# Optimization experiments

Hardware: AMD Instinct MI355X
Metric: run time of the kernel (lower is better)

## Reference

```python
import jax, jax.numpy as jnp
import numpy as np

N_NODES = 100000
N_EDGES = 1600000
N_FEAT = 128
N_CLASSES = 10
N_GRAPHS = 256


def setup_inputs() -> dict:
    key = jax.random.key(0)
    ks = jax.random.split(key, 16)
    x = jax.random.normal(ks[0], (N_NODES, N_FEAT), dtype=jnp.float32)
    edge_index = jax.random.randint(ks[1], (2, N_EDGES), 0, N_NODES, dtype=jnp.int64)
    batch = jnp.sort(jax.random.randint(ks[2], (N_NODES,), 0, N_GRAPHS, dtype=jnp.int64))
    s = 0.1
    # GAT1: in=128 -> heads=8, out_per_head=8, concat -> 64
    W1 = jax.random.normal(ks[3], (N_FEAT, 64), dtype=jnp.float32) * s
    a_src1 = jax.random.normal(ks[4], (8, 8), dtype=jnp.float32) * s
    a_dst1 = jax.random.normal(ks[5], (8, 8), dtype=jnp.float32) * s
    b1 = jnp.zeros((64,), jnp.float32)
    # GAT2: in=64 -> heads=1, out=128
    W2 = jax.random.normal(ks[6], (64, 128), dtype=jnp.float32) * s
    a_src2 = jax.random.normal(ks[7], (1, 128), dtype=jnp.float32) * s
    a_dst2 = jax.random.normal(ks[8], (1, 128), dtype=jnp.float32) * s
    b2 = jnp.zeros((128,), jnp.float32)
    fc_w = jax.random.normal(ks[9], (128, N_CLASSES), dtype=jnp.float32) * s
    fc_b = jnp.zeros((N_CLASSES,), jnp.float32)
    return {"x": x, "edge_index": edge_index, "batch": batch,
            "W1": W1, "a_src1": a_src1, "a_dst1": a_dst1, "b1": b1,
            "W2": W2, "a_src2": a_src2, "a_dst2": a_dst2, "b2": b2,
            "fc_w": fc_w, "fc_b": fc_b}


def _segment_softmax(e, seg, n):
    # e: [E, H]; softmax over edges sharing the same destination node
    m = jax.ops.segment_max(e, seg, num_segments=n)
    m = jnp.where(jnp.isfinite(m), m, jnp.zeros_like(m))  # guard isolated nodes
    ex = jnp.exp(e - m[seg])
    s = jax.ops.segment_sum(ex, seg, num_segments=n)
    return ex / (s[seg] + jnp.asarray(1e-16, e.dtype))


def _gat_conv(x, src, dst, W, a_src, a_dst, bias):
    # PyG GATConv (eval mode, self-loops already appended to src/dst)
    H, C = a_src.shape
    n = x.shape[0]
    h = (x @ W).reshape(n, H, C)                      # [N,H,C]
    al_s = jnp.einsum('nhc,hc->nh', h, a_src)          # [N,H]
    al_d = jnp.einsum('nhc,hc->nh', h, a_dst)
    e = jax.nn.leaky_relu(al_s[src] + al_d[dst], 0.2)  # [E,H]
    alpha = _segment_softmax(e, dst, n)                # [E,H]
    out = jax.ops.segment_sum(h[src] * alpha[..., None], dst, num_segments=n)  # [N,H,C]
    return out.reshape(n, H * C) + bias                # concat=True (H=1 layer2 is identity reshape)


def reference(x, edge_index, batch, W1, a_src1, a_dst1, b1, W2, a_src2, a_dst2, b2, fc_w, fc_b):
    n = x.shape[0]
    loop = jnp.arange(n, dtype=edge_index.dtype)
    src = jnp.concatenate([edge_index[0], loop])       # add self-loops (PyG default)
    dst = jnp.concatenate([edge_index[1], loop])
    x1 = jax.nn.relu(_gat_conv(x, src, dst, W1, a_src1, a_dst1, b1))
    # dropout p=0.6 is identity in eval mode
    x2 = _gat_conv(x1, src, dst, W2, a_src2, a_dst2, b2)
    cnt = jax.ops.segment_sum(jnp.ones((n,), x2.dtype), batch, num_segments=N_GRAPHS)
    pooled = jax.ops.segment_sum(x2, batch, num_segments=N_GRAPHS) / jnp.maximum(cnt, 1.0)[:, None]
    logits = pooled @ fc_w + fc_b
    return jax.nn.log_softmax(logits, axis=1)
```

## Files before the change

kernel.cpp:

```cpp
#include <hip/hip_runtime.h>
#include <math.h>

typedef unsigned int uint;
typedef unsigned short ushort;
typedef unsigned char uchar;
typedef __attribute__((ext_vector_type(2))) float v2f;
typedef __attribute__((ext_vector_type(4))) _Float16 h4v;
typedef __attribute__((ext_vector_type(8))) _Float16 h8v;

#define S1 4.0f
#define S2 16.0f

template <bool HI>
__device__ inline v2f fp8x2f(uint u) {
    return __builtin_amdgcn_cvt_pk_f32_fp8((int)u, HI);
}

__global__ __launch_bounds__(256) void k_g1h(const float* __restrict__ x,
                                             const float* __restrict__ W1,
                                             const float* __restrict__ as1,
                                             const float* __restrict__ ad1,
                                             uchar* __restrict__ rec1,
                                             const int* __restrict__ dst,
                                             int* __restrict__ counts,
                                             int N, int E, int CH, int NB, int GB) {
    __shared__ float sB[128 * 64];
    __shared__ float sA[64 * 68];
    const int t = threadIdx.x;
    if (blockIdx.x >= GB) {
        int b = blockIdx.x - GB;
        int* hist = (int*)sB;
        for (int k = t; k < NB; k += 256) hist[k] = 0;
        __syncthreads();
        int e0 = b * CH;
        int e1 = e0 + CH; if (e1 > E) e1 = E;
        for (int e = e0 + t; e < e1; e += 256)
            atomicAdd(&hist[dst[e] >> 7], 1);
        __syncthreads();
        for (int k = t; k < NB; k += 256) counts[(size_t)b * NB + k] = hist[k];
        return;
    }
    const int n0 = blockIdx.x * 64;
    {
        const float4* w4 = (const float4*)W1;
        float4* s4 = (float4*)sB;
#pragma unroll
        for (int i = 0; i < 8; ++i) s4[t + i * 256] = w4[t + i * 256];
    }
    const int r0 = (t >> 3) * 2;
    const int c0 = (t & 7) * 8;
    float acc0[8] = {0, 0, 0, 0, 0, 0, 0, 0};
    float acc1[8] = {0, 0, 0, 0, 0, 0, 0, 0};
    for (int kb = 0; kb < 2; ++kb) {
        __syncthreads();
#pragma unroll
        for (int i = 0; i < 4; ++i) {
            int idx = t + i * 256;
            int r = idx >> 4, kc = idx & 15;
            int n = n0 + r;
            float4 v = make_float4(0.f, 0.f, 0.f, 0.f);
            if (n < N) v = ((const float4*)x)[(size_t)n * 32 + kb * 16 + kc];
            *(float4*)&sA[r * 68 + kc * 4] = v;
        }
        __syncthreads();
        const float* bptr = &sB[kb * 64 * 64];
#pragma unroll 8
        for (int kk = 0; kk < 64; ++kk) {
            float a0 = sA[r0 * 68 + kk];
            float a1 = sA[(r0 + 1) * 68 + kk];
            const float* bp = &bptr[kk * 64 + c0];
            float4 b0 = *(const float4*)bp;
            float4 b1v = *(const float4*)(bp + 4);
            acc0[0] += a0 * b0.x; acc0[1] += a0 * b0.y; acc0[2] += a0 * b0.z; acc0[3] += a0 * b0.w;
            acc0[4] += a0 * b1v.x; acc0[5] += a0 * b1v.y; acc0[6] += a0 * b1v.z; acc0[7] += a0 * b1v.w;
            acc1[0] += a1 * b0.x; acc1[1] += a1 * b0.y; acc1[2] += a1 * b0.z; acc1[3] += a1 * b0.w;
            acc1[4] += a1 * b1v.x; acc1[5] += a1 * b1v.y; acc1[6] += a1 * b1v.z; acc1[7] += a1 * b1v.w;
        }
    }
    float ps0 = 0.f, pd0 = 0.f, ps1 = 0.f, pd1 = 0.f;
#pragma unroll
    for (int i = 0; i < 8; ++i) {
        float ws = as1[c0 + i], wd = ad1[c0 + i];
        ps0 += acc0[i] * ws; pd0 += acc0[i] * wd;
        ps1 += acc1[i] * ws; pd1 += acc1[i] * wd;
    }
    int n = n0 + r0;
    int head = t & 7;
    if (n < N) {
        int q0 = 0, q1 = 0;
        q0 = __builtin_amdgcn_cvt_pk_fp8_f32(acc0[0] * S1, acc0[1] * S1, q0, false);
        q0 = __builtin_amdgcn_cvt_pk_fp8_f32(acc0[2] * S1, acc0[3] * S1, q0, true);
        q1 = __builtin_amdgcn_cvt_pk_fp8_f32(acc0[4] * S1, acc0[5] * S1, q1, false);
        q1 = __builtin_amdgcn_cvt_pk_fp8_f32(acc0[6] * S1, acc0[7] * S1, q1, true);
        uint2 p; p.x = (uint)q0; p.y = (uint)q1;
        uchar* rp = rec1 + (size_t)n * 128;
        *(uint2*)(rp + c0) = p;
        *(float*)(rp + 64 + head * 4) = ps0;
        *(float*)(rp + 96 + head * 4) = pd0;
    }
    if (n + 1 < N) {
        int q0 = 0, q1 = 0;
        q0 = __builtin_amdgcn_cvt_pk_fp8_f32(acc1[0] * S1, acc1[1] * S1, q0, false);
        q0 = __builtin_amdgcn_cvt_pk_fp8_f32(acc1[2] * S1, acc1[3] * S1, q0, true);
        q1 = __builtin_amdgcn_cvt_pk_fp8_f32(acc1[4] * S1, acc1[5] * S1, q1, false);
        q1 = __builtin_amdgcn_cvt_pk_fp8_f32(acc1[6] * S1, acc1[7] * S1, q1, true);
        uint2 p; p.x = (uint)q0; p.y = (uint)q1;
        uchar* rp = rec1 + (size_t)(n + 1) * 128;
        *(uint2*)(rp + c0) = p;
        *(float*)(rp + 64 + head * 4) = ps1;
        *(float*)(rp + 96 + head * 4) = pd1;
    }
}

__global__ __launch_bounds__(256) void k_gemm2(const _Float16* __restrict__ x1pre,
                                               const float* __restrict__ W2,
                                               const float* __restrict__ b1,
                                               const float* __restrict__ as2,
                                               const float* __restrict__ ad2,
                                               uchar* __restrict__ h2f8,
                                               float* __restrict__ al2s,
                                               float* __restrict__ al2d, int N) {
    __shared__ float sB[64 * 128];
    __shared__ float sA[64 * 68];
    const int t = threadIdx.x;
    const int n0 = blockIdx.x * 64;
    {
        const float4* w4 = (const float4*)W2;
        float4* s4 = (float4*)sB;
#pragma unroll
        for (int i = 0; i < 8; ++i) s4[t + i * 256] = w4[t + i * 256];
    }
#pragma unroll
    for (int i = 0; i < 4; ++i) {
        int idx = t + i * 256;
        int r = idx >> 4, kc = idx & 15;
        int n = n0 + r;
        float4 v = make_float4(0.f, 0.f, 0.f, 0.f);
        if (n < N) {
            h4v hv = *(const h4v*)(x1pre + (size_t)n * 64 + kc * 4);
            float4 bb = ((const float4*)b1)[kc];
            v.x = fmaxf((float)hv[0] + bb.x, 0.f);
            v.y = fmaxf((float)hv[1] + bb.y, 0.f);
            v.z = fmaxf((float)hv[2] + bb.z, 0.f);
            v.w = fmaxf((float)hv[3] + bb.w, 0.f);
        }
        *(float4*)&sA[r * 68 + kc * 4] = v;
    }
    __syncthreads();
    const int r0 = (t >> 3) * 2;
    const int cb = (t & 7) * 4;
    float acc0[16], acc1[16];
#pragma unroll
    for (int i = 0; i < 16; ++i) { acc0[i] = 0.f; acc1[i] = 0.f; }
#pragma unroll 4
    for (int k = 0; k < 64; ++k) {
        float a0 = sA[r0 * 68 + k];
        float a1 = sA[(r0 + 1) * 68 + k];
#pragma unroll
        for (int j = 0; j < 4; ++j) {
            float4 b = *(const float4*)&sB[k * 128 + cb + 32 * j];
            acc0[j * 4 + 0] += a0 * b.x; acc0[j * 4 + 1] += a0 * b.y;
            acc0[j * 4 + 2] += a0 * b.z; acc0[j * 4 + 3] += a0 * b.w;
            acc1[j * 4 + 0] += a1 * b.x; acc1[j * 4 + 1] += a1 * b.y;
            acc1[j * 4 + 2] += a1 * b.z; acc1[j * 4 + 3] += a1 * b.w;
        }
    }
    float ps0 = 0.f, pd0 = 0.f, ps1 = 0.f, pd1 = 0.f;
#pragma unroll
    for (int j = 0; j < 4; ++j)
#pragma unroll
        for (int i = 0; i < 4; ++i) {
            int cc = cb + 32 * j + i;
            float ws = as2[cc], wd = ad2[cc];
            ps0 += acc0[j * 4 + i] * ws; pd0 += acc0[j * 4 + i] * wd;
            ps1 += acc1[j * 4 + i] * ws; pd1 += acc1[j * 4 + i] * wd;
        }
#pragma unroll
    for (int off = 1; off < 8; off <<= 1) {
        ps0 += __shfl_xor(ps0, off); pd0 += __shfl_xor(pd0, off);
        ps1 += __shfl_xor(ps1, off); pd1 += __shfl_xor(pd1, off);
    }
    int n = n0 + r0;
    if (n < N) {
#pragma unroll
        for (int j = 0; j < 4; ++j) {
            int q = 0;
            q = __builtin_amdgcn_cvt_pk_fp8_f32(acc0[j * 4 + 0] * S2, acc0[j * 4 + 1] * S2, q, false);
            q = __builtin_amdgcn_cvt_pk_fp8_f32(acc0[j * 4 + 2] * S2, acc0[j * 4 + 3] * S2, q, true);
            *(uint*)&h2f8[(size_t)n * 128 + cb + 32 * j] = (uint)q;
        }
        if ((t & 7) == 0) { al2s[n] = ps0; al2d[n] = pd0; }
    }
    if (n + 1 < N) {
#pragma unroll
        for (int j = 0; j < 4; ++j) {
            int q = 0;
            q = __builtin_amdgcn_cvt_pk_fp8_f32(acc1[j * 4 + 0] * S2, acc1[j * 4 + 1] * S2, q, false);
            q = __builtin_amdgcn_cvt_pk_fp8_f32(acc1[j * 4 + 2] * S2, acc1[j * 4 + 3] * S2, q, true);
            *(uint*)&h2f8[(size_t)(n + 1) * 128 + cb + 32 * j] = (uint)q;
        }
        if ((t & 7) == 0) { al2s[n + 1] = ps1; al2d[n + 1] = pd1; }
    }
}


__global__ __launch_bounds__(256) void k_bscan(int* __restrict__ counts,
                                               int* __restrict__ btot,
                                               int C, int NB) {
    __shared__ int sh[256];
    int t = threadIdx.x, k = blockIdx.x;
    int v[4];
#pragma unroll
    for (int i = 0; i < 4; ++i) {
        int b = t * 4 + i;
        v[i] = (b < C) ? counts[(size_t)b * NB + k] : 0;
    }
    int s = v[0] + v[1] + v[2] + v[3];
    sh[t] = s;
    __syncthreads();
    int accv = s;
    for (int off = 1; off < 256; off <<= 1) {
        int u = (t >= off) ? sh[t - off] : 0;
        __syncthreads();
        accv += u;
        sh[t] = accv;
        __syncthreads();
    }
    int excl = accv - s;
#pragma unroll
    for (int i = 0; i < 4; ++i) {
        int b = t * 4 + i;
        if (b < C) counts[(size_t)b * NB + k] = excl;
        excl += v[i];
    }
    if (t == 255) btot[k] = accv;
}

__global__ __launch_bounds__(256) void k_bucket(const int* __restrict__ src,
                                                const int* __restrict__ dst,
                                                const int* __restrict__ counts,
                                                const int* __restrict__ btot,
                                                int* __restrict__ bbase,
                                                int* __restrict__ ebuf,
                                                int E, int CH, int NB) {
    __shared__ int pos[784];
    __shared__ int sh[256];
    __shared__ int bb[784];
    int t = threadIdx.x, b = blockIdx.x;
    int v[4];
#pragma unroll
    for (int i = 0; i < 4; ++i) {
        int k = t * 4 + i;
        v[i] = (k < NB) ? btot[k] : 0;
    }
    int s = v[0] + v[1] + v[2] + v[3];
    sh[t] = s;
    __syncthreads();
    int accv = s;
    for (int off = 1; off < 256; off <<= 1) {
        int u = (t >= off) ? sh[t - off] : 0;
        __syncthreads();
        accv += u;
        sh[t] = accv;
        __syncthreads();
    }
    int excl = accv - s;
#pragma unroll
    for (int i = 0; i < 4; ++i) {
        int k = t * 4 + i;
        if (k < NB) bb[k] = excl;
        excl += v[i];
    }
    __syncthreads();
    for (int k = t; k < NB; k += 256)
        pos[k] = bb[k] + counts[(size_t)b * NB + k];
    if (b == 0) {
        for (int k = t; k < NB; k += 256) bbase[k] = bb[k];
        if (t == 0) bbase[NB] = E;
    }
    __syncthreads();
    int e0 = b * CH;
    int e1 = e0 + CH; if (e1 > E) e1 = E;
    for (int e = e0 + t; e < e1; e += 256) {
        int d = dst[e], s2 = src[e];
        int p = atomicAdd(&pos[d >> 7], 1);
        ebuf[p] = (int)((uint)s2 | ((uint)(d & 127) << 25));
    }
}

__global__ __launch_bounds__(256) void k_csr(const int* __restrict__ bbase,
                                             const int* __restrict__ ebuf,
                                             int* __restrict__ row_ptr,
                                             int* __restrict__ col,
                                             int N, int E) {
    __shared__ int cnt[128];
    __shared__ int fill[128];
    __shared__ int rowb[128];
    __shared__ int sh[256];
    int t = threadIdx.x, k = blockIdx.x;
    int lo = bbase[k], hi = bbase[k + 1];
    int nlo = k << 7;
    int nn = N - nlo; if (nn > 128) nn = 128;
    if (t < 128) { cnt[t] = 0; fill[t] = 0; }
    __syncthreads();
    for (int i = lo + t; i < hi; i += 256)
        atomicAdd(&cnt[((uint)ebuf[i]) >> 25], 1);
    __syncthreads();
    int v = (t < nn) ? (cnt[t] + 1) : 0;
    sh[t] = v;
    __syncthreads();
    int accv = v;
    for (int off = 1; off < 256; off <<= 1) {
        int u = (t >= off) ? sh[t - off] : 0;
        __syncthreads();
        accv += u;
        sh[t] = accv;
        __syncthreads();
    }
    int fbase = lo + nlo;
    if (t < nn) {
        int rb = fbase + accv - v;
        rowb[t] = rb;
        row_ptr[nlo + t] = rb;
        col[rb + cnt[t]] = nlo + t;
    }
    if (k == 0 && t == 0) row_ptr[N] = E + N;
    __syncthreads();
    for (int i = lo + t; i < hi; i += 256) {
        uint e = (uint)ebuf[i];
        int j = (int)(e >> 25);
        int r = atomicAdd(&fill[j], 1);
        col[rowb[j] + r] = (int)(e & 0x1FFFFFFu);
    }
}

__global__ __launch_bounds__(256) void k_edge1(const uchar* __restrict__ rec1,
                                               const int* __restrict__ row_ptr,
                                               const int* __restrict__ col,
                                               _Float16* __restrict__ x1pre, int N) {
    int node = blockIdx.x * 4 + (threadIdx.x >> 6);
    if (node >= N) return;
    const int lane = threadIdx.x & 63;
    const int g = lane >> 4;
    const int k4 = lane & 15;
    const int hh = k4 >> 1;
    const uint co = (uint)(k4 * 4);
    const uint ao = 64u + (uint)(hh * 4);
    const float a_dh = *(const float*)(rec1 + (((size_t)node) << 7) + 96 + hh * 4);
    const int s0 = row_ptr[node], s1 = row_ptr[node + 1];
    float den_part = 0.f;
    v2f accL = {0.f, 0.f};
    v2f accH = {0.f, 0.f};
    for (int base = s0; base < s1; base += 64) {
        int cnt = s1 - base; if (cnt > 64) cnt = 64;
        int cntR = (cnt + 3) & ~3;
        int i = 0;
        for (; i + 16 <= cntR; i += 16) {
            int eA = base + i + g, eB = eA + 4, eC = eA + 8, eD = eA + 12;
            int xD = eD < s1 ? eD : s1 - 1;
            int cA = col[eA], cB = col[eB], cC = col[eC], cD = col[xD];
            const uchar* rA = rec1 + (((uint)cA) << 7);
            const uchar* rB = rec1 + (((uint)cB) << 7);
            const uchar* rC = rec1 + (((uint)cC) << 7);
            const uchar* rD = rec1 + (((uint)cD) << 7);
            uint hA = *(const uint*)(rA + co);
            uint hB = *(const uint*)(rB + co);
            uint hC = *(const uint*)(rC + co);
            uint hD = *(const uint*)(rD + co);
            float lA = *(const float*)(rA + ao) + a_dh;
            float lB = *(const float*)(rB + ao) + a_dh;
            float lC = *(const float*)(rC + ao) + a_dh;
            float lD = *(const float*)(rD + ao) + a_dh;
            lA = lA > 0.f ? lA : 0.2f * lA;
            lB = lB > 0.f ? lB : 0.2f * lB;
            lC = lC > 0.f ? lC : 0.2f * lC;
            lD = lD > 0.f ? lD : 0.2f * lD;
            float wA = __expf(lA);
            float wB = __expf(lB);
            float wC = __expf(lC);
            float wD = (eD < s1) ? __expf(lD) : 0.f;
            den_part += wA + wB + wC + wD;
            v2f wA2 = {wA, wA}, wB2 = {wB, wB}, wC2 = {wC, wC}, wD2 = {wD, wD};
            accL += wA2 * fp8x2f<false>(hA);
            accH += wA2 * fp8x2f<true>(hA);
            accL += wB2 * fp8x2f<false>(hB);
            accH += wB2 * fp8x2f<true>(hB);
            accL += wC2 * fp8x2f<false>(hC);
            accH += wC2 * fp8x2f<true>(hC);
            accL += wD2 * fp8x2f<false>(hD);
            accH += wD2 * fp8x2f<true>(hD);
        }
        int rem = cntR - i;
        if (rem & 8) {
            int eA = base + i + g, eB = eA + 4;
            int xB = eB < s1 ? eB : s1 - 1;
            int cA = col[eA], cB = col[xB];
            const uchar* rA = rec1 + (((uint)cA) << 7);
            const uchar* rB = rec1 + (((uint)cB) << 7);
            uint hA = *(const uint*)(rA + co);
            uint hB = *(const uint*)(rB + co);
            float lA = *(const float*)(rA + ao) + a_dh;
            float lB = *(const float*)(rB + ao) + a_dh;
            lA = lA > 0.f ? lA : 0.2f * lA;
            lB = lB > 0.f ? lB : 0.2f * lB;
            float wA = __expf(lA);
            float wB = (eB < s1) ? __expf(lB) : 0.f;
            den_part += wA + wB;
            v2f wA2 = {wA, wA}, wB2 = {wB, wB};
            accL += wA2 * fp8x2f<false>(hA);
            accH += wA2 * fp8x2f<true>(hA);
            accL += wB2 * fp8x2f<false>(hB);
            accH += wB2 * fp8x2f<true>(hB);
            i += 8;
        }
        if (rem & 4) {
            int eA = base + i + g;
            int xA = eA < s1 ? eA : s1 - 1;
            int cA = col[xA];
            const uchar* rA = rec1 + (((uint)cA) << 7);
            uint hA = *(const uint*)(rA + co);
            float lA = *(const float*)(rA + ao) + a_dh;
            lA = lA > 0.f ? lA : 0.2f * lA;
            float wA = (eA < s1) ? __expf(lA) : 0.f;
            den_part += wA;
            v2f wA2 = {wA, wA};
            accL += wA2 * fp8x2f<false>(hA);
            accH += wA2 * fp8x2f<true>(hA);
        }
    }
    float a0 = accL.x, a1 = accL.y, a2 = accH.x, a3 = accH.y;
    a0 += __shfl_xor(a0, 16); a0 += __shfl_xor(a0, 32);
    a1 += __shfl_xor(a1, 16); a1 += __shfl_xor(a1, 32);
    a2 += __shfl_xor(a2, 16); a2 += __shfl_xor(a2, 32);
    a3 += __shfl_xor(a3, 16); a3 += __shfl_xor(a3, 32);
    den_part += __shfl_xor(den_part, 16);
    den_part += __shfl_xor(den_part, 32);
    if (lane < 16) {
        float invd = 1.f / (den_part * S1);
        h4v o;
        o[0] = (_Float16)(a0 * invd);
        o[1] = (_Float16)(a1 * invd);
        o[2] = (_Float16)(a2 * invd);
        o[3] = (_Float16)(a3 * invd);
        *(h4v*)(x1pre + (size_t)node * 64 + co) = o;
    }
}

__global__ __launch_bounds__(256) void k_edge2(const uchar* __restrict__ h2f8,
                                               const float* __restrict__ al2s,
                                               const float* __restrict__ al2d,
                                               const int* __restrict__ row_ptr,
                                               const int* __restrict__ col,
                                               _Float16* __restrict__ x2, int N) {
    int node = blockIdx.x * 4 + (threadIdx.x >> 6);
    if (node >= N) return;
    const int lane = threadIdx.x & 63;
    const int g = lane >> 4;
    const int k8 = lane & 15;
    const uint co = (uint)(k8 * 8);
    const float a_d = al2d[node];
    const int s0 = row_ptr[node], s1 = row_ptr[node + 1];
    v2f acc0 = {0.f, 0.f}, acc1 = {0.f, 0.f}, acc2 = {0.f, 0.f}, acc3 = {0.f, 0.f};
    float den_part = 0.f;
    for (int base = s0; base < s1; base += 64) {
        int cnt = s1 - base; if (cnt > 64) cnt = 64;
        int cntR = (cnt + 3) & ~3;
        int i = 0;
        for (; i + 16 <= cntR; i += 16) {
            int eA = base + i + g, eB = eA + 4, eC = eA + 8, eD = eA + 12;
            int xD = eD < s1 ? eD : s1 - 1;
            int cA = col[eA], cB = col[eB], cC = col[eC], cD = col[xD];
            uint2 hA = *(const uint2*)(h2f8 + ((((uint)cA) << 7) | co));
            uint2 hB = *(const uint2*)(h2f8 + ((((uint)cB) << 7) | co));
            uint2 hC = *(const uint2*)(h2f8 + ((((uint)cC) << 7) | co));
            uint2 hD = *(const uint2*)(h2f8 + ((((uint)cD) << 7) | co));
            float lA = al2s[(uint)cA] + a_d;
            float lB = al2s[(uint)cB] + a_d;
            float lC = al2s[(uint)cC] + a_d;
            float lD = al2s[(uint)cD] + a_d;
            lA = lA > 0.f ? lA : 0.2f * lA;
            lB = lB > 0.f ? lB : 0.2f * lB;
            lC = lC > 0.f ? lC : 0.2f * lC;
            lD = lD > 0.f ? lD : 0.2f * lD;
            float wA = __expf(lA);
            float wB = __expf(lB);
            float wC = __expf(lC);
            float wD = (eD < s1) ? __expf(lD) : 0.f;
            den_part += wA + wB + wC + wD;
            v2f wA2 = {wA, wA}, wB2 = {wB, wB}, wC2 = {wC, wC}, wD2 = {wD, wD};
            acc0 += wA2 * fp8x2f<false>(hA.x);
            acc1 += wA2 * fp8x2f<true>(hA.x);
            acc2 += wA2 * fp8x2f<false>(hA.y);
            acc3 += wA2 * fp8x2f<true>(hA.y);
            acc0 += wB2 * fp8x2f<false>(hB.x);
            acc1 += wB2 * fp8x2f<true>(hB.x);
            acc2 += wB2 * fp8x2f<false>(hB.y);
            acc3 += wB2 * fp8x2f<true>(hB.y);
            acc0 += wC2 * fp8x2f<false>(hC.x);
            acc1 += wC2 * fp8x2f<true>(hC.x);
            acc2 += wC2 * fp8x2f<false>(hC.y);
            acc3 += wC2 * fp8x2f<true>(hC.y);
            acc0 += wD2 * fp8x2f<false>(hD.x);
            acc1 += wD2 * fp8x2f<true>(hD.x);
            acc2 += wD2 * fp8x2f<false>(hD.y);
            acc3 += wD2 * fp8x2f<true>(hD.y);
        }
        int rem = cntR - i;
        if (rem & 8) {
            int eA = base + i + g, eB = eA + 4;
            int xB = eB < s1 ? eB : s1 - 1;
            int cA = col[eA], cB = col[xB];
            uint2 hA = *(const uint2*)(h2f8 + ((((uint)cA) << 7) | co));
            uint2 hB = *(const uint2*)(h2f8 + ((((uint)cB) << 7) | co));
            float lA = al2s[(uint)cA] + a_d;
            float lB = al2s[(uint)cB] + a_d;
            lA = lA > 0.f ? lA : 0.2f * lA;
            lB = lB > 0.f ? lB : 0.2f * lB;
            float wA = __expf(lA);
            float wB = (eB < s1) ? __expf(lB) : 0.f;
            den_part += wA + wB;
            v2f wA2 = {wA, wA}, wB2 = {wB, wB};
            acc0 += wA2 * fp8x2f<false>(hA.x);
            acc1 += wA2 * fp8x2f<true>(hA.x);
            acc2 += wA2 * fp8x2f<false>(hA.y);
            acc3 += wA2 * fp8x2f<true>(hA.y);
            acc0 += wB2 * fp8x2f<false>(hB.x);
            acc1 += wB2 * fp8x2f<true>(hB.x);
            acc2 += wB2 * fp8x2f<false>(hB.y);
            acc3 += wB2 * fp8x2f<true>(hB.y);
            i += 8;
        }
        if (rem & 4) {
            int eA = base + i + g;
            int xA = eA < s1 ? eA : s1 - 1;
            int cA = col[xA];
            uint2 hA = *(const uint2*)(h2f8 + ((((uint)cA) << 7) | co));
            float lA = al2s[(uint)cA] + a_d;
            lA = lA > 0.f ? lA : 0.2f * lA;
            float wA = (eA < s1) ? __expf(lA) : 0.f;
            den_part += wA;
            v2f wA2 = {wA, wA};
            acc0 += wA2 * fp8x2f<false>(hA.x);
            acc1 += wA2 * fp8x2f<true>(hA.x);
            acc2 += wA2 * fp8x2f<false>(hA.y);
            acc3 += wA2 * fp8x2f<true>(hA.y);
        }
    }
    den_part += __shfl_xor(den_part, 16);
    den_part += __shfl_xor(den_part, 32);
    float r0 = acc0.x, r1 = acc0.y, r2 = acc1.x, r3 = acc1.y;
    float r4 = acc2.x, r5 = acc2.y, r6 = acc3.x, r7 = acc3.y;
    r0 += __shfl_xor(r0, 16); r0 += __shfl_xor(r0, 32);
    r1 += __shfl_xor(r1, 16); r1 += __shfl_xor(r1, 32);
    r2 += __shfl_xor(r2, 16); r2 += __shfl_xor(r2, 32);
    r3 += __shfl_xor(r3, 16); r3 += __shfl_xor(r3, 32);
    r4 += __shfl_xor(r4, 16); r4 += __shfl_xor(r4, 32);
    r5 += __shfl_xor(r5, 16); r5 += __shfl_xor(r5, 32);
    r6 += __shfl_xor(r6, 16); r6 += __shfl_xor(r6, 32);
    r7 += __shfl_xor(r7, 16); r7 += __shfl_xor(r7, 32);
    if (lane < 16) {
        float invd = 1.f / (den_part * S2);
        h8v o;
        o[0] = (_Float16)(r0 * invd);
        o[1] = (_Float16)(r1 * invd);
        o[2] = (_Float16)(r2 * invd);
        o[3] = (_Float16)(r3 * invd);
        o[4] = (_Float16)(r4 * invd);
        o[5] = (_Float16)(r5 * invd);
        o[6] = (_Float16)(r6 * invd);
        o[7] = (_Float16)(r7 * invd);
        *(h8v*)(x2 + (size_t)node * 128 + co) = o;
    }
}

__global__ __launch_bounds__(128) void k_poolfc(const _Float16* __restrict__ x2,
                                                const int* __restrict__ batch,
                                                const float* __restrict__ b2,
                                                const float* __restrict__ fcw,
                                                const float* __restrict__ fcb,
                                                float* __restrict__ out,
                                                int N, int G) {
    __shared__ float sp[128];
    const int g = blockIdx.x;
    const int t = threadIdx.x;
    int lo = 0, hi = N;
    while (lo < hi) { int m = (lo + hi) >> 1; if (batch[m] < g) lo = m + 1; else hi = m; }
    const int s = lo;
    hi = N;
    while (lo < hi) { int m = (lo + hi) >> 1; if (batch[m] < g + 1) lo = m + 1; else hi = m; }
    const int e = lo;
    float a0 = 0.f, a1 = 0.f, a2 = 0.f, a3 = 0.f;
    int n = s;
    for (; n + 4 <= e; n += 4) {
        a0 += (float)x2[(size_t)(n + 0) * 128 + t];
        a1 += (float)x2[(size_t)(n + 1) * 128 + t];
        a2 += (float)x2[(size_t)(n + 2) * 128 + t];
        a3 += (float)x2[(size_t)(n + 3) * 128 + t];
    }
    for (; n < e; ++n) a0 += (float)x2[(size_t)n * 128 + t];
    float inv = 1.f / fmaxf((float)(e - s), 1.f);
    sp[t] = (a0 + a1 + a2 + a3) * inv + b2[t];
    __syncthreads();
    if (t < 64) {
        int c = t;
        float2 p = ((const float2*)sp)[c];
        float l[10];
#pragma unroll
        for (int j = 0; j < 10; ++j)
            l[j] = p.x * fcw[(2 * c) * 10 + j] + p.y * fcw[(2 * c + 1) * 10 + j];
#pragma unroll
        for (int j = 0; j < 10; ++j)
            for (int off = 1; off < 64; off <<= 1) l[j] += __shfl_xor(l[j], off);
        if (c == 0) {
            float lj[10];
            float m = -1e30f;
#pragma unroll
            for (int j = 0; j < 10; ++j) {
                lj[j] = l[j] + fcb[j];
                m = fmaxf(m, lj[j]);
            }
            float sde = 0.f;
#pragma unroll
            for (int j = 0; j < 10; ++j) sde += expf(lj[j] - m);
            float ls = logf(sde);
#pragma unroll
            for (int j = 0; j < 10; ++j) out[(size_t)g * 10 + j] = lj[j] - m - ls;
        }
    }
}

extern "C" void kernel_launch(void* const* d_in, const int* in_sizes, int n_in,
                              void* d_out, int out_size, void* d_ws, size_t ws_size,
                              hipStream_t stream) {
    const float* x     = (const float*)d_in[0];
    const int*   ei    = (const int*)d_in[1];
    const int*   batch = (const int*)d_in[2];
    const float* W1    = (const float*)d_in[3];
    const float* as1   = (const float*)d_in[4];
    const float* ad1   = (const float*)d_in[5];
    const float* b1    = (const float*)d_in[6];
    const float* W2    = (const float*)d_in[7];
    const float* as2   = (const float*)d_in[8];
    const float* ad2   = (const float*)d_in[9];
    const float* b2    = (const float*)d_in[10];
    const float* fcw   = (const float*)d_in[11];
    const float* fcb   = (const float*)d_in[12];
    float* out = (float*)d_out;

    const int N = in_sizes[0] / 128;
    const int E = in_sizes[1] / 2;
    const int G = out_size / 10;
    const int* srcp = ei;
    const int* dstp = ei + E;

    float* wf = (float*)d_ws;
    uchar*    rec1  = (uchar*)wf;
    _Float16* x1pre = (_Float16*)(wf + (size_t)N * 32);
    _Float16* x2    = (_Float16*)wf;
    uchar*    h2f8  = (uchar*)(wf + (size_t)N * 128);
    float* al2s_  = wf + (size_t)N * 176;
    float* al2d_  = wf + (size_t)N * 177;

    const int NB = (N + 127) >> 7;
    const int C  = 1024;
    const int CH = (E + C - 1) / C;

    int* ib = (int*)(((uintptr_t)(wf + (size_t)N * 178) + 15) & ~(uintptr_t)15);
    int* ebuf    = ib;
    int* counts  = ib + (size_t)E;
    int* btot    = counts + (size_t)C * NB;
    int* bbase   = btot + NB;
    int* row_ptr = bbase + NB + 1;
    int* col     = row_ptr + N + 1;

    const int nb64 = (N + 63) / 64;
    const int nb4  = (N + 3) / 4;

    k_g1h<<<nb64 + C, 256, 0, stream>>>(x, W1, as1, ad1, rec1, dstp, counts,
                                        N, E, CH, NB, nb64);
    k_bscan<<<NB, 256, 0, stream>>>(counts, btot, C, NB);
    k_bucket<<<C, 256, 0, stream>>>(srcp, dstp, counts, btot, bbase, ebuf, E, CH, NB);
    k_csr<<<NB, 256, 0, stream>>>(bbase, ebuf, row_ptr, col, N, E);
    k_edge1<<<nb4, 256, 0, stream>>>(rec1, row_ptr, col, x1pre, N);
    k_gemm2<<<nb64, 256, 0, stream>>>(x1pre, W2, b1, as2, ad2, h2f8, al2s_, al2d_, N);
    k_edge2<<<nb4, 256, 0, stream>>>(h2f8, al2s_, al2d_, row_ptr, col, x2, N);
    k_poolfc<<<G, 128, 0, stream>>>(x2, batch, b2, fcw, fcb, out, N, G);
}
```

Before: 343.9 us.

## Store layer-2 features as fp16 and accumulate edge2 with packed fp16 math

Layer-2 node features are now stored as fp16 instead of scaled fp8. The edge2 aggregation accumulates with packed 8-wide fp16 multiply-adds instead of fp8-to-fp32 conversions plus fp32 FMAs. This removes the per-element fp8 unpack work but doubles the gather bytes per neighbor and accumulates in fp16, which risks precision loss. Separately, the bucket-count constant C drops from 1024 to 256, which changes the CSR build parallelism.

```diff
diff --git a/kernel.cpp b/kernel.cpp
--- a/kernel.cpp
+++ b/kernel.cpp
@@ -9,7 +9,6 @@
 typedef __attribute__((ext_vector_type(8))) _Float16 h8v;
 
 #define S1 4.0f
-#define S2 16.0f
 
 template <bool HI>
 __device__ inline v2f fp8x2f(uint u) {
@@ -117,7 +116,7 @@
                                                const float* __restrict__ b1,
                                                const float* __restrict__ as2,
                                                const float* __restrict__ ad2,
-                                               uchar* __restrict__ h2f8,
+                                               _Float16* __restrict__ h2,
                                                float* __restrict__ al2s,
                                                float* __restrict__ al2d, int N) {
     __shared__ float sB[64 * 128];
@@ -184,20 +183,24 @@
     if (n < N) {
 #pragma unroll
         for (int j = 0; j < 4; ++j) {
-            int q = 0;
-            q = __builtin_amdgcn_cvt_pk_fp8_f32(acc0[j * 4 + 0] * S2, acc0[j * 4 + 1] * S2, q, false);
-            q = __builtin_amdgcn_cvt_pk_fp8_f32(acc0[j * 4 + 2] * S2, acc0[j * 4 + 3] * S2, q, true);
-            *(uint*)&h2f8[(size_t)n * 128 + cb + 32 * j] = (uint)q;
+            h4v o;
+            o[0] = (_Float16)acc0[j * 4 + 0];
+            o[1] = (_Float16)acc0[j * 4 + 1];
+            o[2] = (_Float16)acc0[j * 4 + 2];
+            o[3] = (_Float16)acc0[j * 4 + 3];
+            *(h4v*)&h2[(size_t)n * 128 + cb + 32 * j] = o;
         }
         if ((t & 7) == 0) { al2s[n] = ps0; al2d[n] = pd0; }
     }
     if (n + 1 < N) {
 #pragma unroll
         for (int j = 0; j < 4; ++j) {
-            int q = 0;
-            q = __builtin_amdgcn_cvt_pk_fp8_f32(acc1[j * 4 + 0] * S2, acc1[j * 4 + 1] * S2, q, false);
-            q = __builtin_amdgcn_cvt_pk_fp8_f32(acc1[j * 4 + 2] * S2, acc1[j * 4 + 3] * S2, q, true);
-            *(uint*)&h2f8[(size_t)(n + 1) * 128 + cb + 32 * j] = (uint)q;
+            h4v o;
+            o[0] = (_Float16)acc1[j * 4 + 0];
+            o[1] = (_Float16)acc1[j * 4 + 1];
+            o[2] = (_Float16)acc1[j * 4 + 2];
+            o[3] = (_Float16)acc1[j * 4 + 3];
+            *(h4v*)&h2[(size_t)(n + 1) * 128 + cb + 32 * j] = o;
         }
         if ((t & 7) == 0) { al2s[n + 1] = ps1; al2d[n + 1] = pd1; }
     }
@@ -446,7 +449,7 @@
     }
 }
 
-__global__ __launch_bounds__(256) void k_edge2(const uchar* __restrict__ h2f8,
+__global__ __launch_bounds__(256) void k_edge2(const _Float16* __restrict__ h2,
                                                const float* __restrict__ al2s,
                                                const float* __restrict__ al2d,
                                                const int* __restrict__ row_ptr,
@@ -460,7 +463,8 @@
     const uint co = (uint)(k8 * 8);
     const float a_d = al2d[node];
     const int s0 = row_ptr[node], s1 = row_ptr[node + 1];
-    v2f acc0 = {0.f, 0.f}, acc1 = {0.f, 0.f}, acc2 = {0.f, 0.f}, acc3 = {0.f, 0.f};
+    h8v acc8 = {(_Float16)0.f, (_Float16)0.f, (_Float16)0.f, (_Float16)0.f,
+                (_Float16)0.f, (_Float16)0.f, (_Float16)0.f, (_Float16)0.f};
     float den_part = 0.f;
     for (int base = s0; base < s1; base += 64) {
         int cnt = s1 - base; if (cnt > 64) cnt = 64;
@@ -470,10 +474,10 @@
             int eA = base + i + g, eB = eA + 4, eC = eA + 8, eD = eA + 12;
             int xD = eD < s1 ? eD : s1 - 1;
             int cA = col[eA], cB = col[eB], cC = col[eC], cD = col[xD];
-            uint2 hA = *(const uint2*)(h2f8 + ((((uint)cA) << 7) | co));
-            uint2 hB = *(const uint2*)(h2f8 + ((((uint)cB) << 7) | co));
-            uint2 hC = *(const uint2*)(h2f8 + ((((uint)cC) << 7) | co));
-            uint2 hD = *(const uint2*)(h2f8 + ((((uint)cD) << 7) | co));
+            h8v hA = *(const h8v*)(h2 + ((((size_t)(uint)cA) << 7) + co));
+            h8v hB = *(const h8v*)(h2 + ((((size_t)(uint)cB) << 7) + co));
+            h8v hC = *(const h8v*)(h2 + ((((size_t)(uint)cC) << 7) + co));
+            h8v hD = *(const h8v*)(h2 + ((((size_t)(uint)cD) << 7) + co));
             float lA = al2s[(uint)cA] + a_d;
             float lB = al2s[(uint)cB] + a_d;
             float lC = al2s[(uint)cC] + a_d;
@@ -487,31 +491,24 @@
             float wC = __expf(lC);
             float wD = (eD < s1) ? __expf(lD) : 0.f;
             den_part += wA + wB + wC + wD;
-            v2f wA2 = {wA, wA}, wB2 = {wB, wB}, wC2 = {wC, wC}, wD2 = {wD, wD};
-            acc0 += wA2 * fp8x2f<false>(hA.x);
-            acc1 += wA2 * fp8x2f<true>(hA.x);
-            acc2 += wA2 * fp8x2f<false>(hA.y);
-            acc3 += wA2 * fp8x2f<true>(hA.y);
-            acc0 += wB2 * fp8x2f<false>(hB.x);
-            acc1 += wB2 * fp8x2f<true>(hB.x);
-            acc2 += wB2 * fp8x2f<false>(hB.y);
-            acc3 += wB2 * fp8x2f<true>(hB.y);
-            acc0 += wC2 * fp8x2f<false>(hC.x);
-            acc1 += wC2 * fp8x2f<true>(hC.x);
-            acc2 += wC2 * fp8x2f<false>(hC.y);
-            acc3 += wC2 * fp8x2f<true>(hC.y);
-            acc0 += wD2 * fp8x2f<false>(hD.x);
-            acc1 += wD2 * fp8x2f<true>(hD.x);
-            acc2 += wD2 * fp8x2f<false>(hD.y);
-            acc3 += wD2 * fp8x2f<true>(hD.y);
+            _Float16 fA = (_Float16)wA, fB = (_Float16)wB;
+            _Float16 fC = (_Float16)wC, fD = (_Float16)wD;
+            h8v wA8 = {fA, fA, fA, fA, fA, fA, fA, fA};
+            h8v wB8 = {fB, fB, fB, fB, fB, fB, fB, fB};
+            h8v wC8 = {fC, fC, fC, fC, fC, fC, fC, fC};
+            h8v wD8 = {fD, fD, fD, fD, fD, fD, fD, fD};
+            acc8 += hA * wA8;
+            acc8 += hB * wB8;
+            acc8 += hC * wC8;
+            acc8 += hD * wD8;
         }
         int rem = cntR - i;
         if (rem & 8) {
             int eA = base + i + g, eB = eA + 4;
             int xB = eB < s1 ? eB : s1 - 1;
             int cA = col[eA], cB = col[xB];
-            uint2 hA = *(const uint2*)(h2f8 + ((((uint)cA) << 7) | co));
-            uint2 hB = *(const uint2*)(h2f8 + ((((uint)cB) << 7) | co));
+            h8v hA = *(const h8v*)(h2 + ((((size_t)(uint)cA) << 7) + co));
+            h8v hB = *(const h8v*)(h2 + ((((size_t)(uint)cB) << 7) + co));
             float lA = al2s[(uint)cA] + a_d;
             float lB = al2s[(uint)cB] + a_d;
             lA = lA > 0.f ? lA : 0.2f * lA;
@@ -519,37 +516,31 @@
             float wA = __expf(lA);
             float wB = (eB < s1) ? __expf(lB) : 0.f;
             den_part += wA + wB;
-            v2f wA2 = {wA, wA}, wB2 = {wB, wB};
-            acc0 += wA2 * fp8x2f<false>(hA.x);
-            acc1 += wA2 * fp8x2f<true>(hA.x);
-            acc2 += wA2 * fp8x2f<false>(hA.y);
-            acc3 += wA2 * fp8x2f<true>(hA.y);
-            acc0 += wB2 * fp8x2f<false>(hB.x);
-            acc1 += wB2 * fp8x2f<true>(hB.x);
-            acc2 += wB2 * fp8x2f<false>(hB.y);
-            acc3 += wB2 * fp8x2f<true>(hB.y);
+            _Float16 fA = (_Float16)wA, fB = (_Float16)wB;
+            h8v wA8 = {fA, fA, fA, fA, fA, fA, fA, fA};
+            h8v wB8 = {fB, fB, fB, fB, fB, fB, fB, fB};
+            acc8 += hA * wA8;
+            acc8 += hB * wB8;
             i += 8;
         }
         if (rem & 4) {
             int eA = base + i + g;
             int xA = eA < s1 ? eA : s1 - 1;
             int cA = col[xA];
-            uint2 hA = *(const uint2*)(h2f8 + ((((uint)cA) << 7) | co));
+            h8v hA = *(const h8v*)(h2 + ((((size_t)(uint)cA) << 7) + co));
             float lA = al2s[(uint)cA] + a_d;
             lA = lA > 0.f ? lA : 0.2f * lA;
             float wA = (eA < s1) ? __expf(lA) : 0.f;
             den_part += wA;
-            v2f wA2 = {wA, wA};
-            acc0 += wA2 * fp8x2f<false>(hA.x);
-            acc1 += wA2 * fp8x2f<true>(hA.x);
-            acc2 += wA2 * fp8x2f<false>(hA.y);
-            acc3 += wA2 * fp8x2f<true>(hA.y);
+            _Float16 fA = (_Float16)wA;
+            h8v wA8 = {fA, fA, fA, fA, fA, fA, fA, fA};
+            acc8 += hA * wA8;
         }
     }
     den_part += __shfl_xor(den_part, 16);
     den_part += __shfl_xor(den_part, 32);
-    float r0 = acc0.x, r1 = acc0.y, r2 = acc1.x, r3 = acc1.y;
-    float r4 = acc2.x, r5 = acc2.y, r6 = acc3.x, r7 = acc3.y;
+    float r0 = (float)acc8[0], r1 = (float)acc8[1], r2 = (float)acc8[2], r3 = (float)acc8[3];
+    float r4 = (float)acc8[4], r5 = (float)acc8[5], r6 = (float)acc8[6], r7 = (float)acc8[7];
     r0 += __shfl_xor(r0, 16); r0 += __shfl_xor(r0, 32);
     r1 += __shfl_xor(r1, 16); r1 += __shfl_xor(r1, 32);
     r2 += __shfl_xor(r2, 16); r2 += __shfl_xor(r2, 32);
@@ -559,7 +550,7 @@
     r6 += __shfl_xor(r6, 16); r6 += __shfl_xor(r6, 32);
     r7 += __shfl_xor(r7, 16); r7 += __shfl_xor(r7, 32);
     if (lane < 16) {
-        float invd = 1.f / (den_part * S2);
+        float invd = 1.f / den_part;
         h8v o;
         o[0] = (_Float16)(r0 * invd);
         o[1] = (_Float16)(r1 * invd);
@@ -657,15 +648,15 @@
     uchar*    rec1  = (uchar*)wf;
     _Float16* x1pre = (_Float16*)(wf + (size_t)N * 32);
     _Float16* x2    = (_Float16*)wf;
-    uchar*    h2f8  = (uchar*)(wf + (size_t)N * 128);
-    float* al2s_  = wf + (size_t)N * 176;
-    float* al2d_  = wf + (size_t)N * 177;
+    _Float16* h2    = (_Float16*)(wf + (size_t)N * 128);
+    float* al2s_  = wf + (size_t)N * 192;
+    float* al2d_  = wf + (size_t)N * 193;
 
     const int NB = (N + 127) >> 7;
-    const int C  = 1024;
+    const int C  = 256;
     const int CH = (E + C - 1) / C;
 
-    int* ib = (int*)(((uintptr_t)(wf + (size_t)N * 178) + 15) & ~(uintptr_t)15);
+    int* ib = (int*)(((uintptr_t)(wf + (size_t)N * 194) + 15) & ~(uintptr_t)15);
     int* ebuf    = ib;
     int* counts  = ib + (size_t)E;
     int* btot    = counts + (size_t)C * NB;
@@ -682,7 +673,7 @@
     k_bucket<<<C, 256, 0, stream>>>(srcp, dstp, counts, btot, bbase, ebuf, E, CH, NB);
     k_csr<<<NB, 256, 0, stream>>>(bbase, ebuf, row_ptr, col, N, E);
     k_edge1<<<nb4, 256, 0, stream>>>(rec1, row_ptr, col, x1pre, N);
-    k_gemm2<<<nb64, 256, 0, stream>>>(x1pre, W2, b1, as2, ad2, h2f8, al2s_, al2d_, N);
-    k_edge2<<<nb4, 256, 0, stream>>>(h2f8, al2s_, al2d_, row_ptr, col, x2, N);
+    k_gemm2<<<nb64, 256, 0, stream>>>(x1pre, W2, b1, as2, ad2, h2, al2s_, al2d_, N);
+    k_edge2<<<nb4, 256, 0, stream>>>(h2, al2s_, al2d_, row_ptr, col, x2, N);
     k_poolfc<<<G, 128, 0, stream>>>(x2, batch, b2, fcw, fcb, out, N, G);
 }
```

Result: no change. 348.8 us (+1.4%).
